# Kernel optimization log

Measured on AMD Instinct MI355X. Metric: run time of the kernel, lower is better.

The kernel has to match this reference:

```python
import jax, jax.numpy as jnp
import numpy as np

IGNORE = 255


def setup_inputs() -> dict:
    key = jax.random.key(0)
    k1, k2 = jax.random.split(key)
    B, C, H, W = 4, 19, 512, 1024
    logits = jax.random.normal(k1, (B, C, H, W), dtype=jnp.float32)
    label = jax.random.randint(k2, (B, H, W), 0, 20)
    # map the out-of-range class 19 to the ignore index 255 (as hard-coded in forward)
    label = jnp.where(label == 19, IGNORE, label).astype(jnp.int64)
    return {"logits": logits, "label": label}


def _lovasz_softmax(logits, label):
    # logits: [B,C,H,W] float32, label: [B,H,W] int
    B, C, H, W = logits.shape
    probs = jax.nn.softmax(logits, axis=1)                      # [B,C,H,W]
    probs_flat = probs.transpose(0, 2, 3, 1).reshape(-1, C)     # [N,C]
    lab = label.reshape(-1)                                     # [N]
    valid = lab != IGNORE

    def per_class(c):
        fg = ((lab == c) & valid).astype(probs_flat.dtype)      # [N]
        # ignored pixels get zero error -> sorted last, contribute 0 to the loss
        err = jnp.where(valid, jnp.abs(fg - probs_flat[:, c]), 0.0)
        order = jnp.argsort(-err)                               # descending errors
        err_s = err[order]
        fg_s = fg[order]
        gts = fg_s.sum()
        inter = gts - jnp.cumsum(fg_s)
        union = gts + jnp.cumsum(1.0 - fg_s)
        jacc = 1.0 - inter / union                              # Lovász extension of Jaccard
        grad = jnp.concatenate([jacc[:1], jacc[1:] - jacc[:-1]])
        return jnp.dot(err_s, grad)

    losses = jax.vmap(per_class)(jnp.arange(C))                 # [C]
    return losses.sum()


def reference(logits, label):
    return _lovasz_softmax(logits.astype(jnp.float32), label)
```

## Files before the change

kernel.cpp:

```cpp
#include <hip/hip_runtime.h>

#define C_CLS 19
#define NBINS 128
#define NREP 8
#define ROWSTRIDE (NBINS * NREP + 1)
#define HW_SHIFT 19
#define HW (1 << HW_SHIFT)
#define NPIX (4 * HW)
#define IGNORE_LAB 255

__global__ __launch_bounds__(512) void lovasz_hist(
    const float* __restrict__ logits, const int* __restrict__ label,
    unsigned long long* __restrict__ g_hist)
{
    __shared__ unsigned hist[C_CLS * ROWSTRIDE];
    for (int i = threadIdx.x; i < C_CLS * ROWSTRIDE; i += blockDim.x) hist[i] = 0u;
    __syncthreads();

    const int rep = threadIdx.x & (NREP - 1);
    const int npairs = NPIX / 2;
    const int stride = gridDim.x * blockDim.x;
    for (int pr = blockIdx.x * blockDim.x + threadIdx.x; pr < npairs; pr += stride) {
        const long long p = (long long)pr * 2;
        const int b  = (int)(p >> HW_SHIFT);
        const int hw = (int)(p & (HW - 1));
        const float* base = logits + ((long long)b * C_CLS << HW_SHIFT) + hw;

        float2 e[C_CLS];
        float sx = 0.f, sy = 0.f;
        #pragma unroll
        for (int c = 0; c < C_CLS; ++c) {
            float2 v = *(const float2*)(base + ((long long)c << HW_SHIFT));
            const float ex = __expf(v.x);
            const float ey = __expf(v.y);
            e[c].x = ex; e[c].y = ey;
            sx += ex; sy += ey;
        }
        const float rxN = (float)NBINS / sx;
        const float ryN = (float)NBINS / sy;

        const int2 lab = *(const int2*)(label + p);
        const bool v0 = (lab.x != IGNORE_LAB);
        const bool v1 = (lab.y != IGNORE_LAB);

        #pragma unroll
        for (int c = 0; c < C_CLS; ++c) {
            const int rowbase = c * ROWSTRIDE + rep;
            if (v0) {
                int it = (int)(e[c].x * rxN);
                it = it > (NBINS - 1) ? (NBINS - 1) : it;
                const bool fg = (lab.x == c);
                const int bin = fg ? (NBINS - 1 - it) : it;
                atomicAdd(&hist[rowbase + (bin << 3)], fg ? 0x10001u : 0x10000u);
            }
            if (v1) {
                int it = (int)(e[c].y * ryN);
                it = it > (NBINS - 1) ? (NBINS - 1) : it;
                const bool fg = (lab.y == c);
                const int bin = fg ? (NBINS - 1 - it) : it;
                atomicAdd(&hist[rowbase + (bin << 3)], fg ? 0x10001u : 0x10000u);
            }
        }
    }
    __syncthreads();

    for (int e = threadIdx.x; e < C_CLS * NBINS; e += blockDim.x) {
        const int c = e >> 7;
        const int b = e & (NBINS - 1);
        const int base = c * ROWSTRIDE + (b << 3);
        unsigned v = 0;
        #pragma unroll
        for (int r = 0; r < NREP; ++r) v += hist[base + r];
        if (v) {
            const unsigned long long add =
                ((unsigned long long)(v >> 16) << 32) | (unsigned long long)(v & 0xFFFFu);
            atomicAdd(&g_hist[e], add);
        }
    }
}

__global__ __launch_bounds__(512) void lovasz_finalize(
    const unsigned long long* __restrict__ g_hist, float* __restrict__ out)
{
    __shared__ double partial[8];
    const int wave = threadIdx.x >> 6;
    const int lane = threadIdx.x & 63;
    const int PER = NBINS / 64;

    double acc = 0.0;
    for (int c = wave; c < C_CLS; c += 8) {
        unsigned n[PER], f[PER];
        unsigned nl = 0, fl = 0;
        #pragma unroll
        for (int k = 0; k < PER; ++k) {
            const int s = lane * PER + k;
            const int bin = NBINS - 1 - s;
            const unsigned long long h = g_hist[c * NBINS + bin];
            n[k] = (unsigned)(h >> 32);
            f[k] = (unsigned)(h & 0xFFFFFFFFull);
            nl += n[k]; fl += f[k];
        }

        unsigned ni = nl, fi = fl;
        for (int off = 1; off < 64; off <<= 1) {
            const unsigned nn = __shfl_up(ni, off);
            const unsigned ff = __shfl_up(fi, off);
            if (lane >= off) { ni += nn; fi += ff; }
        }
        const unsigned gts = __shfl(fi, 63);

        unsigned Tc = ni - nl;
        unsigned Fc = fi - fl;

        double term = 0.0;
        {
            const unsigned den = gts + Tc - Fc;
            double Jprev = den ? 1.0 - (double)(gts - Fc) / (double)den : 0.0;
            #pragma unroll
            for (int k = 0; k < PER; ++k) {
                if (n[k]) {
                    Tc += n[k]; Fc += f[k];
                    const unsigned d1 = gts + Tc - Fc;
                    const double J = d1 ? 1.0 - (double)(gts - Fc) / (double)d1 : 0.0;
                    const int s = lane * PER + k;
                    const double center = ((double)(NBINS - 1 - s) + 0.5) / (double)NBINS;
                    term += center * (J - Jprev);
                    Jprev = J;
                }
            }
        }
        for (int off = 32; off > 0; off >>= 1) term += __shfl_down(term, off);
        if (lane == 0) acc += term;
    }

    if (lane == 0) partial[wave] = acc;
    __syncthreads();
    if (threadIdx.x == 0) {
        double s = 0.0;
        #pragma unroll
        for (int w = 0; w < 8; ++w) s += partial[w];
        out[0] = (float)s;
    }
}

extern "C" void kernel_launch(void* const* d_in, const int* in_sizes, int n_in,
                              void* d_out, int out_size, void* d_ws, size_t ws_size,
                              hipStream_t stream) {
    const float* logits = (const float*)d_in[0];
    const int*   label  = (const int*)d_in[1];
    unsigned long long* g_hist = (unsigned long long*)d_ws;

    hipMemsetAsync(d_ws, 0, (size_t)C_CLS * NBINS * sizeof(unsigned long long), stream);

    lovasz_hist<<<512, 512, 0, stream>>>(logits, label, g_hist);
    lovasz_finalize<<<1, 512, 0, stream>>>(g_hist, (float*)d_out);
}
```

Before: 51.33 us.

## Replace grid-stride pixel loop with one float4 quad per thread

The histogram kernel no longer uses a grid-stride loop over pixel pairs. Each thread now handles exactly four consecutive pixels with float4 logit loads and an int4 label load, and the grid is doubled to 1024 blocks so the whole image is covered in one pass. The aim is wider memory transactions, less loop overhead and more loads in flight. In exchange, register pressure rises with 19 float4 values held per thread. Each block also pays the full shared-histogram zeroing and global flush while processing half as many pixels as before, so that per-block cost doubles in total.

```diff
diff --git a/kernel.cpp b/kernel.cpp
--- a/kernel.cpp
+++ b/kernel.cpp
@@ -18,63 +18,78 @@
     __syncthreads();
 
     const int rep = threadIdx.x & (NREP - 1);
-    const int npairs = NPIX / 2;
-    const int stride = gridDim.x * blockDim.x;
-    for (int pr = blockIdx.x * blockDim.x + threadIdx.x; pr < npairs; pr += stride) {
-        const long long p = (long long)pr * 2;
-        const int b  = (int)(p >> HW_SHIFT);
-        const int hw = (int)(p & (HW - 1));
-        const float* base = logits + ((long long)b * C_CLS << HW_SHIFT) + hw;
+    const int t = blockIdx.x * blockDim.x + threadIdx.x;
+    const long long p = (long long)t * 4;
+    const int b  = (int)(p >> HW_SHIFT);
+    const int hw = (int)(p & (HW - 1));
+    const float* base = logits + ((long long)b * C_CLS << HW_SHIFT) + hw;
 
-        float2 e[C_CLS];
-        float sx = 0.f, sy = 0.f;
-        #pragma unroll
-        for (int c = 0; c < C_CLS; ++c) {
-            float2 v = *(const float2*)(base + ((long long)c << HW_SHIFT));
-            const float ex = __expf(v.x);
-            const float ey = __expf(v.y);
-            e[c].x = ex; e[c].y = ey;
-            sx += ex; sy += ey;
+    float4 e[C_CLS];
+    float s0 = 0.f, s1 = 0.f, s2 = 0.f, s3 = 0.f;
+    #pragma unroll
+    for (int c = 0; c < C_CLS; ++c) {
+        float4 v = *(const float4*)(base + ((long long)c << HW_SHIFT));
+        v.x = __expf(v.x); v.y = __expf(v.y);
+        v.z = __expf(v.z); v.w = __expf(v.w);
+        e[c] = v;
+        s0 += v.x; s1 += v.y; s2 += v.z; s3 += v.w;
+    }
+    const float r0 = (float)NBINS / s0;
+    const float r1 = (float)NBINS / s1;
+    const float r2 = (float)NBINS / s2;
+    const float r3 = (float)NBINS / s3;
+
+    const int4 lab = *(const int4*)(label + p);
+    const bool va = (lab.x != IGNORE_LAB);
+    const bool vb = (lab.y != IGNORE_LAB);
+    const bool vc = (lab.z != IGNORE_LAB);
+    const bool vd = (lab.w != IGNORE_LAB);
+
+    #pragma unroll
+    for (int c = 0; c < C_CLS; ++c) {
+        const int rowbase = c * ROWSTRIDE + rep;
+        if (va) {
+            int it = (int)(e[c].x * r0);
+            it = it > (NBINS - 1) ? (NBINS - 1) : it;
+            const bool fg = (lab.x == c);
+            const int bin = fg ? (NBINS - 1 - it) : it;
+            atomicAdd(&hist[rowbase + (bin << 3)], fg ? 0x10001u : 0x10000u);
         }
-        const float rxN = (float)NBINS / sx;
-        const float ryN = (float)NBINS / sy;
-
-        const int2 lab = *(const int2*)(label + p);
-        const bool v0 = (lab.x != IGNORE_LAB);
-        const bool v1 = (lab.y != IGNORE_LAB);
-
-        #pragma unroll
-        for (int c = 0; c < C_CLS; ++c) {
-            const int rowbase = c * ROWSTRIDE + rep;
-            if (v0) {
-                int it = (int)(e[c].x * rxN);
-                it = it > (NBINS - 1) ? (NBINS - 1) : it;
-                const bool fg = (lab.x == c);
-                const int bin = fg ? (NBINS - 1 - it) : it;
-                atomicAdd(&hist[rowbase + (bin << 3)], fg ? 0x10001u : 0x10000u);
-            }
-            if (v1) {
-                int it = (int)(e[c].y * ryN);
-                it = it > (NBINS - 1) ? (NBINS - 1) : it;
-                const bool fg = (lab.y == c);
-                const int bin = fg ? (NBINS - 1 - it) : it;
-                atomicAdd(&hist[rowbase + (bin << 3)], fg ? 0x10001u : 0x10000u);
-            }
+        if (vb) {
+            int it = (int)(e[c].y * r1);
+            it = it > (NBINS - 1) ? (NBINS - 1) : it;
+            const bool fg = (lab.y == c);
+            const int bin = fg ? (NBINS - 1 - it) : it;
+            atomicAdd(&hist[rowbase + (bin << 3)], fg ? 0x10001u : 0x10000u);
+        }
+        if (vc) {
+            int it = (int)(e[c].z * r2);
+            it = it > (NBINS - 1) ? (NBINS - 1) : it;
+            const bool fg = (lab.z == c);
+            const int bin = fg ? (NBINS - 1 - it) : it;
+            atomicAdd(&hist[rowbase + (bin << 3)], fg ? 0x10001u : 0x10000u);
+        }
+        if (vd) {
+            int it = (int)(e[c].w * r3);
+            it = it > (NBINS - 1) ? (NBINS - 1) : it;
+            const bool fg = (lab.w == c);
+            const int bin = fg ? (NBINS - 1 - it) : it;
+            atomicAdd(&hist[rowbase + (bin << 3)], fg ? 0x10001u : 0x10000u);
         }
     }
     __syncthreads();
 
-    for (int e = threadIdx.x; e < C_CLS * NBINS; e += blockDim.x) {
-        const int c = e >> 7;
-        const int b = e & (NBINS - 1);
-        const int base = c * ROWSTRIDE + (b << 3);
+    for (int e2 = threadIdx.x; e2 < C_CLS * NBINS; e2 += blockDim.x) {
+        const int c = e2 >> 7;
+        const int bn = e2 & (NBINS - 1);
+        const int base2 = c * ROWSTRIDE + (bn << 3);
         unsigned v = 0;
         #pragma unroll
-        for (int r = 0; r < NREP; ++r) v += hist[base + r];
+        for (int r = 0; r < NREP; ++r) v += hist[base2 + r];
         if (v) {
             const unsigned long long add =
                 ((unsigned long long)(v >> 16) << 32) | (unsigned long long)(v & 0xFFFFu);
-            atomicAdd(&g_hist[e], add);
+            atomicAdd(&g_hist[e2], add);
         }
     }
 }
@@ -152,6 +167,6 @@
 
     hipMemsetAsync(d_ws, 0, (size_t)C_CLS * NBINS * sizeof(unsigned long long), stream);
 
-    lovasz_hist<<<512, 512, 0, stream>>>(logits, label, g_hist);
+    lovasz_hist<<<1024, 512, 0, stream>>>(logits, label, g_hist);
     lovasz_finalize<<<1, 512, 0, stream>>>(g_hist, (float*)d_out);
 }
```

Measured after the change: 55.07 us. +7.3%, slower.
